# Kernel optimization log

Hardware: AMD Instinct MI355X
Metric: run time of the kernel (lower is better)

## Reference

```python
import jax, jax.numpy as jnp
import numpy as np

ALPHA = 0.2  # LeakyReLU negative slope


def setup_inputs() -> dict:
    key = jax.random.key(0)
    ks = jax.random.split(key, 7)
    B, Wn, K, E, O = 16, 64, 256, 128, 64
    s = lambda k, shape, fan: jax.random.normal(k, shape, jnp.float32) * (1.0 / np.sqrt(fan))
    return {
        "x": jax.random.normal(ks[0], (B, Wn, K), jnp.float32),
        "lin_w": s(ks[1], (E, 2 * Wn), 2 * Wn),   # torch Linear weight (out,in)
        "lin_b": jnp.zeros((E,), jnp.float32),
        "a": s(ks[2], (E,), E),
        "bias_kk": s(ks[3], (K, K), K) * 0.1,
        "fc_w": s(ks[4], (O, K), K),
        "fc_b": jnp.zeros((O,), jnp.float32),
    }


def reference(x, lin_w, lin_b, a, bias_kk, fc_w, fc_b):
    # x: (B, W, K) -> v: (B, K, W); K nodes, W features per node
    v = jnp.transpose(x, (0, 2, 1))
    Wn = v.shape[-1]
    # lin(concat(v_i, v_j)) == v_i @ W1^T + v_j @ W2^T + b  (avoids O(K^2*2W) concat)
    W1, W2 = lin_w[:, :Wn], lin_w[:, Wn:]
    left = jnp.einsum("bkw,ew->bke", v, W1)   # (B,K,E)
    right = jnp.einsum("bkw,ew->bke", v, W2)  # (B,K,E)
    g = left[:, :, None, :] + right[:, None, :, :] + lin_b  # (B,K,K,E)
    g = jnp.where(g >= 0, g, ALPHA * g)  # LeakyReLU
    e = jnp.einsum("bije,e->bij", g, a) + bias_kk  # (B,K,K)
    attn = jax.nn.softmax(e, axis=2)
    # dropout p=0.0 / eval mode -> identity
    h = jax.nn.sigmoid(jnp.einsum("bij,bjw->biw", attn, v))  # (B,K,W)
    out = jnp.einsum("bwk,ok->bwo", jnp.transpose(h, (0, 2, 1)), fc_w) + fc_b
    return out  # (B, W, out_dim)
```

## Files before the change

### kernel.cpp

```cpp
#include <hip/hip_runtime.h>
#include <hip/hip_bf16.h>

#define ALPHA 0.2f
#define C1 0.6f
#define C2 0.4f

__global__ __launch_bounds__(256) void k_proj(
    const float* __restrict__ x, const float* __restrict__ lin_w,
    float* __restrict__ left, float* __restrict__ right, float* __restrict__ v) {
  const int xcd = blockIdx.x & 7;
  const int s   = blockIdx.x >> 3;
  const int b   = 2 * xcd + (s & 1);
  const int k0  = (s >> 1) * 8;
  const int tid = threadIdx.x;

  __shared__ float s_x[8][68];

  {
    const int w  = tid >> 2;
    const int kq = tid & 3;
    float2 xv = *(const float2*)(x + b * 16384 + w * 256 + k0 + kq * 2);
    s_x[kq * 2 + 0][w] = xv.x;
    s_x[kq * 2 + 1][w] = xv.y;
  }
  __syncthreads();

  if (tid < 128) {
    const int k  = tid >> 4;
    const int wq = tid & 15;
    float4 vv = *(const float4*)&s_x[k][wq * 4];
    *(float4*)(v + (b * 256 + k0 + k) * 64 + wq * 4) = vv;
  }

  const int e  = tid & 127;
  const int kh = tid >> 7;
  float accL[4] = {0, 0, 0, 0};
  float accR[4] = {0, 0, 0, 0};
  const float4* w1 = (const float4*)(lin_w + e * 128);
  const float4* w2 = w1 + 16;
#pragma unroll
  for (int wc = 0; wc < 16; ++wc) {
    float4 l = w1[wc];
    float4 r = w2[wc];
#pragma unroll
    for (int k = 0; k < 4; ++k) {
      float4 sx = *(const float4*)&s_x[kh * 4 + k][wc * 4];
      accL[k] += sx.x * l.x + sx.y * l.y + sx.z * l.z + sx.w * l.w;
      accR[k] += sx.x * r.x + sx.y * r.y + sx.z * r.z + sx.w * r.w;
    }
  }
#pragma unroll
  for (int k = 0; k < 4; ++k) {
    int kk = (b * 256 + k0 + kh * 4 + k) * 128 + e;
    left[kk]  = accL[k];
    right[kk] = accR[k];
  }
}

__global__ __launch_bounds__(256) void k_attn(
    const float* __restrict__ left, const float* __restrict__ right,
    const float* __restrict__ lin_b, const float* __restrict__ a,
    const float* __restrict__ bias_kk, const float* __restrict__ v,
    float* __restrict__ h) {
  const int xcd = blockIdx.x & 7;
  const int sblk = blockIdx.x >> 3;
  const int b   = 2 * xcd + (sblk & 1);
  const int i0  = (sblk >> 1) * 8;
  const int tid = threadIdx.x;

  __shared__ float s_lb[8][132];
  __shared__ float s_a[128];
  __shared__ float s_ca[128];
  __shared__ float s_AL[8];
  __shared__ float s_sc[8][260];
  __shared__ float s_inv[8];
  __shared__ float s_v[128][68];

  float bk[8];
#pragma unroll
  for (int i = 0; i < 8; ++i) bk[i] = bias_kk[(i0 + i) * 256 + tid];

  if (tid < 128) {
    float av = a[tid];
    s_a[tid]  = av;
    s_ca[tid] = C2 * av;
  }
  {
    const int ii = tid >> 5;
    const int e4 = (tid & 31) * 4;
    float4 lv = *(const float4*)(left + (b * 256 + i0 + ii) * 128 + e4);
    float4 bv = *(const float4*)(lin_b + e4);
    lv.x += bv.x; lv.y += bv.y; lv.z += bv.z; lv.w += bv.w;
    *(float4*)&s_lb[ii][e4] = lv;
  }
  __syncthreads();

  {
    const int ii = tid >> 5, sl = tid & 31;
    float p = 0.f;
#pragma unroll
    for (int m = 0; m < 4; ++m) p += s_a[sl * 4 + m] * s_lb[ii][sl * 4 + m];
#pragma unroll
    for (int off = 16; off > 0; off >>= 1) p += __shfl_xor(p, off, 64);
    if (sl == 0) s_AL[ii] = p;
  }

  float acc[8];
#pragma unroll
  for (int i = 0; i < 8; ++i) acc[i] = 0.f;
  float ar = 0.f;
  const float4* rp = (const float4*)(right + (b * 256 + tid) * 128);
#pragma unroll
  for (int ec = 0; ec < 8; ++ec) {
    float4 r0 = rp[ec * 4 + 0], r1 = rp[ec * 4 + 1],
           r2 = rp[ec * 4 + 2], r3 = rp[ec * 4 + 3];
    float4 a0 = *(const float4*)&s_a[ec * 16 + 0];
    float4 a1 = *(const float4*)&s_a[ec * 16 + 4];
    float4 a2 = *(const float4*)&s_a[ec * 16 + 8];
    float4 a3 = *(const float4*)&s_a[ec * 16 + 12];
    ar += a0.x * r0.x + a0.y * r0.y + a0.z * r0.z + a0.w * r0.w;
    ar += a1.x * r1.x + a1.y * r1.y + a1.z * r1.z + a1.w * r1.w;
    ar += a2.x * r2.x + a2.y * r2.y + a2.z * r2.z + a2.w * r2.w;
    ar += a3.x * r3.x + a3.y * r3.y + a3.z * r3.z + a3.w * r3.w;
    float4 c0 = *(const float4*)&s_ca[ec * 16 + 0];
    float4 c1 = *(const float4*)&s_ca[ec * 16 + 4];
    float4 c2 = *(const float4*)&s_ca[ec * 16 + 8];
    float4 c3 = *(const float4*)&s_ca[ec * 16 + 12];
#pragma unroll
    for (int i = 0; i < 8; ++i) {
      float4 l0 = *(const float4*)&s_lb[i][ec * 16 + 0];
      float4 l1 = *(const float4*)&s_lb[i][ec * 16 + 4];
      float4 l2 = *(const float4*)&s_lb[i][ec * 16 + 8];
      float4 l3 = *(const float4*)&s_lb[i][ec * 16 + 12];
      float t, s = acc[i];
      t = l0.x + r0.x; s = fmaf(c0.x, fabsf(t), s);
      t = l0.y + r0.y; s = fmaf(c0.y, fabsf(t), s);
      t = l0.z + r0.z; s = fmaf(c0.z, fabsf(t), s);
      t = l0.w + r0.w; s = fmaf(c0.w, fabsf(t), s);
      t = l1.x + r1.x; s = fmaf(c1.x, fabsf(t), s);
      t = l1.y + r1.y; s = fmaf(c1.y, fabsf(t), s);
      t = l1.z + r1.z; s = fmaf(c1.z, fabsf(t), s);
      t = l1.w + r1.w; s = fmaf(c1.w, fabsf(t), s);
      t = l2.x + r2.x; s = fmaf(c2.x, fabsf(t), s);
      t = l2.y + r2.y; s = fmaf(c2.y, fabsf(t), s);
      t = l2.z + r2.z; s = fmaf(c2.z, fabsf(t), s);
      t = l2.w + r2.w; s = fmaf(c2.w, fabsf(t), s);
      t = l3.x + r3.x; s = fmaf(c3.x, fabsf(t), s);
      t = l3.y + r3.y; s = fmaf(c3.y, fabsf(t), s);
      t = l3.z + r3.z; s = fmaf(c3.z, fabsf(t), s);
      t = l3.w + r3.w; s = fmaf(c3.w, fabsf(t), s);
      acc[i] = s;
    }
  }
  __syncthreads();

#pragma unroll
  for (int i = 0; i < 8; ++i) {
    float sc = fmaf(C1, s_AL[i] + ar, acc[i]) + bk[i];
    s_sc[i][tid] = __expf(sc);
  }
  __syncthreads();

  {
    const int wv = tid >> 6, lane = tid & 63;
#pragma unroll
    for (int rr = 0; rr < 2; ++rr) {
      int i = wv * 2 + rr;
      float s = s_sc[i][lane] + s_sc[i][lane + 64] +
                s_sc[i][lane + 128] + s_sc[i][lane + 192];
#pragma unroll
      for (int off = 32; off > 0; off >>= 1) s += __shfl_xor(s, off, 64);
      if (lane == 0) s_inv[i] = 1.f / s;
    }
  }

  const int iq = tid >> 5;
  const int w  = (tid & 31) * 2;
  float h0 = 0.f, h1 = 0.f;
#pragma unroll
  for (int c = 0; c < 2; ++c) {
    __syncthreads();
#pragma unroll
    for (int t = 0; t < 8; ++t) {
      int idx = tid + t * 256;
      int row = idx >> 4, col = (idx & 15) * 4;
      *(float4*)&s_v[row][col] =
          *(const float4*)(v + (b * 256 + c * 128 + row) * 64 + col);
    }
    __syncthreads();
#pragma unroll 4
    for (int jj = 0; jj < 128; jj += 4) {
      float4 at = *(const float4*)&s_sc[iq][c * 128 + jj];
      float2 v0 = *(const float2*)&s_v[jj + 0][w];
      float2 v1 = *(const float2*)&s_v[jj + 1][w];
      float2 v2 = *(const float2*)&s_v[jj + 2][w];
      float2 v3 = *(const float2*)&s_v[jj + 3][w];
      h0 += at.x * v0.x + at.y * v1.x + at.z * v2.x + at.w * v3.x;
      h1 += at.x * v0.y + at.y * v1.y + at.z * v2.y + at.w * v3.y;
    }
  }
  float inv = s_inv[iq];
  float2 hv;
  hv.x = 1.f / (1.f + __expf(-h0 * inv));
  hv.y = 1.f / (1.f + __expf(-h1 * inv));
  *(float2*)(h + (b * 256 + i0 + iq) * 64 + w) = hv;
}

__global__ __launch_bounds__(256) void k_out(
    const float* __restrict__ h, const float* __restrict__ fc_w,
    const float* __restrict__ fc_b, float* __restrict__ out) {
  const int xcd = blockIdx.x & 7;
  const int s   = blockIdx.x >> 3;
  const int b   = 2 * xcd + (s & 1);
  const int wg  = s >> 1;
  const int wl  = threadIdx.x >> 6;
  const int o   = threadIdx.x & 63;
  const int w   = wg * 4 + wl;

  __shared__ float s_h[256 * 4];
  for (int idx = threadIdx.x; idx < 1024; idx += 256) {
    int k = idx >> 2, wl2 = idx & 3;
    s_h[idx] = h[(b * 256 + k) * 64 + wg * 4 + wl2];
  }
  __syncthreads();

  float acc = 0.f;
  const float4* fw = (const float4*)(fc_w + o * 256);
#pragma unroll
  for (int k4 = 0; k4 < 64; ++k4) {
    float4 f = fw[k4];
    int k = k4 * 4;
    acc += s_h[(k + 0) * 4 + wl] * f.x + s_h[(k + 1) * 4 + wl] * f.y +
           s_h[(k + 2) * 4 + wl] * f.z + s_h[(k + 3) * 4 + wl] * f.w;
  }
  out[b * 64 * 64 + w * 64 + o] = acc + fc_b[o];
}

extern "C" void kernel_launch(void* const* d_in, const int* in_sizes, int n_in,
                              void* d_out, int out_size, void* d_ws, size_t ws_size,
                              hipStream_t stream) {
  const float* x       = (const float*)d_in[0];
  const float* lin_w   = (const float*)d_in[1];
  const float* lin_b   = (const float*)d_in[2];
  const float* a       = (const float*)d_in[3];
  const float* bias_kk = (const float*)d_in[4];
  const float* fc_w    = (const float*)d_in[5];
  const float* fc_b    = (const float*)d_in[6];
  float* out = (float*)d_out;

  float* ws    = (float*)d_ws;
  float* left  = ws;
  float* right = ws + 524288;
  float* v     = ws + 1048576;
  float* h     = ws + 1310720;

  k_proj<<<512, 256, 0, stream>>>(x, lin_w, left, right, v);
  k_attn<<<512, 256, 0, stream>>>(left, right, lin_b, a, bias_kk, v, h);
  k_out<<<256, 256, 0, stream>>>(h, fc_w, fc_b, out);
}
```

Baseline: 104.2 us.

## Halve rows per attention block and double the grid to 1024 blocks

Result: slower. 111.7 us (+7.1%).

```diff
diff --git a/kernel.cpp b/kernel.cpp
--- a/kernel.cpp
+++ b/kernel.cpp
@@ -62,30 +62,30 @@
     const float* __restrict__ lin_b, const float* __restrict__ a,
     const float* __restrict__ bias_kk, const float* __restrict__ v,
     float* __restrict__ h) {
-  const int xcd = blockIdx.x & 7;
+  const int xcd  = blockIdx.x & 7;
   const int sblk = blockIdx.x >> 3;
-  const int b   = 2 * xcd + (sblk & 1);
-  const int i0  = (sblk >> 1) * 8;
-  const int tid = threadIdx.x;
-
-  __shared__ float s_lb[8][132];
+  const int b    = 2 * xcd + (sblk & 1);
+  const int i0   = (sblk >> 1) * 4;
+  const int tid  = threadIdx.x;
+
+  __shared__ float s_lb[4][132];
   __shared__ float s_a[128];
   __shared__ float s_ca[128];
-  __shared__ float s_AL[8];
-  __shared__ float s_sc[8][260];
-  __shared__ float s_inv[8];
-  __shared__ float s_v[128][68];
-
-  float bk[8];
-#pragma unroll
-  for (int i = 0; i < 8; ++i) bk[i] = bias_kk[(i0 + i) * 256 + tid];
+  __shared__ float s_AL[4];
+  __shared__ float s_sc[4][260];
+  __shared__ float s_inv[4];
+  __shared__ float s_v[64][68];
+
+  float bk[4];
+#pragma unroll
+  for (int i = 0; i < 4; ++i) bk[i] = bias_kk[(i0 + i) * 256 + tid];
 
   if (tid < 128) {
     float av = a[tid];
     s_a[tid]  = av;
     s_ca[tid] = C2 * av;
   }
-  {
+  if (tid < 128) {
     const int ii = tid >> 5;
     const int e4 = (tid & 31) * 4;
     float4 lv = *(const float4*)(left + (b * 256 + i0 + ii) * 128 + e4);
@@ -95,7 +95,7 @@
   }
   __syncthreads();
 
-  {
+  if (tid < 128) {
     const int ii = tid >> 5, sl = tid & 31;
     float p = 0.f;
 #pragma unroll
@@ -105,9 +105,7 @@
     if (sl == 0) s_AL[ii] = p;
   }
 
-  float acc[8];
-#pragma unroll
-  for (int i = 0; i < 8; ++i) acc[i] = 0.f;
+  float acc[4] = {0.f, 0.f, 0.f, 0.f};
   float ar = 0.f;
   const float4* rp = (const float4*)(right + (b * 256 + tid) * 128);
 #pragma unroll
@@ -127,7 +125,7 @@
     float4 c2 = *(const float4*)&s_ca[ec * 16 + 8];
     float4 c3 = *(const float4*)&s_ca[ec * 16 + 12];
 #pragma unroll
-    for (int i = 0; i < 8; ++i) {
+    for (int i = 0; i < 4; ++i) {
       float4 l0 = *(const float4*)&s_lb[i][ec * 16 + 0];
       float4 l1 = *(const float4*)&s_lb[i][ec * 16 + 4];
       float4 l2 = *(const float4*)&s_lb[i][ec * 16 + 8];
@@ -155,7 +153,7 @@
   __syncthreads();
 
 #pragma unroll
-  for (int i = 0; i < 8; ++i) {
+  for (int i = 0; i < 4; ++i) {
     float sc = fmaf(C1, s_AL[i] + ar, acc[i]) + bk[i];
     s_sc[i][tid] = __expf(sc);
   }
@@ -163,47 +161,35 @@
 
   {
     const int wv = tid >> 6, lane = tid & 63;
-#pragma unroll
-    for (int rr = 0; rr < 2; ++rr) {
-      int i = wv * 2 + rr;
-      float s = s_sc[i][lane] + s_sc[i][lane + 64] +
-                s_sc[i][lane + 128] + s_sc[i][lane + 192];
-#pragma unroll
-      for (int off = 32; off > 0; off >>= 1) s += __shfl_xor(s, off, 64);
-      if (lane == 0) s_inv[i] = 1.f / s;
-    }
-  }
-
-  const int iq = tid >> 5;
-  const int w  = (tid & 31) * 2;
-  float h0 = 0.f, h1 = 0.f;
-#pragma unroll
-  for (int c = 0; c < 2; ++c) {
+    float s = s_sc[wv][lane] + s_sc[wv][lane + 64] +
+              s_sc[wv][lane + 128] + s_sc[wv][lane + 192];
+#pragma unroll
+    for (int off = 32; off > 0; off >>= 1) s += __shfl_xor(s, off, 64);
+    if (lane == 0) s_inv[wv] = 1.f / s;
+  }
+
+  const int iq = tid >> 6;
+  const int w  = tid & 63;
+  float h0 = 0.f;
+#pragma unroll
+  for (int c = 0; c < 4; ++c) {
     __syncthreads();
 #pragma unroll
-    for (int t = 0; t < 8; ++t) {
+    for (int t = 0; t < 4; ++t) {
       int idx = tid + t * 256;
       int row = idx >> 4, col = (idx & 15) * 4;
       *(float4*)&s_v[row][col] =
-          *(const float4*)(v + (b * 256 + c * 128 + row) * 64 + col);
+          *(const float4*)(v + (b * 256 + c * 64 + row) * 64 + col);
     }
     __syncthreads();
 #pragma unroll 4
-    for (int jj = 0; jj < 128; jj += 4) {
-      float4 at = *(const float4*)&s_sc[iq][c * 128 + jj];
-      float2 v0 = *(const float2*)&s_v[jj + 0][w];
-      float2 v1 = *(const float2*)&s_v[jj + 1][w];
-      float2 v2 = *(const float2*)&s_v[jj + 2][w];
-      float2 v3 = *(const float2*)&s_v[jj + 3][w];
-      h0 += at.x * v0.x + at.y * v1.x + at.z * v2.x + at.w * v3.x;
-      h1 += at.x * v0.y + at.y * v1.y + at.z * v2.y + at.w * v3.y;
-    }
-  }
-  float inv = s_inv[iq];
-  float2 hv;
-  hv.x = 1.f / (1.f + __expf(-h0 * inv));
-  hv.y = 1.f / (1.f + __expf(-h1 * inv));
-  *(float2*)(h + (b * 256 + i0 + iq) * 64 + w) = hv;
+    for (int jj = 0; jj < 64; jj += 4) {
+      float4 at = *(const float4*)&s_sc[iq][c * 64 + jj];
+      h0 += at.x * s_v[jj + 0][w] + at.y * s_v[jj + 1][w] +
+            at.z * s_v[jj + 2][w] + at.w * s_v[jj + 3][w];
+    }
+  }
+  h[(b * 256 + i0 + iq) * 64 + w] = 1.f / (1.f + __expf(-h0 * s_inv[iq]));
 }
 
 __global__ __launch_bounds__(256) void k_out(
@@ -255,6 +241,6 @@
   float* h     = ws + 1310720;
 
   k_proj<<<512, 256, 0, stream>>>(x, lin_w, left, right, v);
-  k_attn<<<512, 256, 0, stream>>>(left, right, lin_b, a, bias_kk, v, h);
+  k_attn<<<1024, 256, 0, stream>>>(left, right, lin_b, a, bias_kk, v, h);
   k_out<<<256, 256, 0, stream>>>(h, fc_w, fc_b, out);
 }
```
